# Kernel optimization log

Hardware: AMD Instinct MI355X
Metric: run time of the kernel (lower is better)

Reference implementation:

```python
import jax, jax.numpy as jnp
import numpy as np

TAU = 2.0
BN_EPS = 1e-5
SG_ALPHA = 4.0  # spikingjelly default sigmoid surrogate alpha

@jax.custom_vjp
def heaviside(x):
    return (x >= 0).astype(x.dtype)

def _h_fwd(x):
    return heaviside(x), x

def _h_bwd(x, g):
    sg = jax.nn.sigmoid(SG_ALPHA * x)
    return (SG_ALPHA * sg * (1.0 - sg) * g,)

heaviside.defvjp(_h_fwd, _h_bwd)

def lif(x, v_th):
    # x: (T, ...). LIFNode defaults: tau=2, decay_input=True, v_reset=0 (hard reset).
    def step(v, xt):
        v = v + (xt - v) / TAU
        s = heaviside(v - v_th)
        return v * (1.0 - s), s
    _, spikes = jax.lax.scan(step, jnp.zeros_like(x[0]), x)
    return spikes

def bn(x, gamma, beta, mean, var):
    # x: (T,B,D,V), channel axis = 2; inference-mode BatchNorm1d
    inv = gamma * jax.lax.rsqrt(var + BN_EPS)
    return x * inv[None, None, :, None] + (beta - mean * inv)[None, None, :, None]

def conv1x1(W, x):
    # W: (out,in), x: (T,B,D,V)
    return jnp.einsum('od,tbdv->tbov', W, x)

def setup_inputs() -> dict:
    key = jax.random.key(0)
    T, B, D, V = 4, 64, 512, 256
    ks = jax.random.split(key, 4)
    s = 1.0 / np.sqrt(D)
    return {
        'x': jax.random.normal(ks[0], (T, B, D, V), jnp.float32),
        'Wq': jax.random.normal(ks[1], (D, D), jnp.float32) * s,
        'q_gamma': jnp.ones((D,), jnp.float32), 'q_beta': jnp.zeros((D,), jnp.float32),
        'q_mean': jnp.zeros((D,), jnp.float32), 'q_var': jnp.ones((D,), jnp.float32),
        'Wk': jax.random.normal(ks[2], (D, D), jnp.float32) * s,
        'k_gamma': jnp.ones((D,), jnp.float32), 'k_beta': jnp.zeros((D,), jnp.float32),
        'k_mean': jnp.zeros((D,), jnp.float32), 'k_var': jnp.ones((D,), jnp.float32),
        'Wp': jax.random.normal(ks[3], (D, D), jnp.float32) * s,
        'p_gamma': jnp.ones((D,), jnp.float32), 'p_beta': jnp.zeros((D,), jnp.float32),
        'p_mean': jnp.zeros((D,), jnp.float32), 'p_var': jnp.ones((D,), jnp.float32),
    }

def reference(x, Wq, q_gamma, q_beta, q_mean, q_var,
              Wk, k_gamma, k_beta, k_mean, k_var,
              Wp, p_gamma, p_beta, p_mean, p_var):
    T, B, D, V = x.shape
    H = 4
    hd = D // H
    q = lif(bn(conv1x1(Wq, x), q_gamma, q_beta, q_mean, q_var), 1.0)
    k = lif(bn(conv1x1(Wk, x), k_gamma, k_beta, k_mean, k_var), 1.0)
    qh = q.reshape(T, B, H, hd, V)
    kh = k.reshape(T, B, H, hd, V)
    q_sum = qh.sum(axis=3, keepdims=True)        # (T,B,H,1,V)
    gate = lif(q_sum, 0.5)                        # attn_lif, threshold 0.5
    out = (gate * kh).reshape(T, B, D, V)
    out2 = lif(bn(conv1x1(Wp, out), p_gamma, p_beta, p_mean, p_var), 1.0)
    return out2
```

## Files before the change

### kernel.cpp

```cpp
#include <hip/hip_runtime.h>

#define T_ 4
#define B_ 64
#define D_ 512
#define V_ 256

#define XSH   0ull
#define XSM   67108864ull
#define XSL   134217728ull
#define OUTBT 201326592ull
#define WT    268435456ull
#define BNOF  273154048ull

typedef unsigned short u16;
typedef __attribute__((ext_vector_type(8))) __bf16 bf16x8;
typedef __attribute__((ext_vector_type(4))) float f32x4;
typedef __attribute__((ext_vector_type(8))) unsigned short u16x8;
typedef __attribute__((ext_vector_type(4))) unsigned short u16x4;

__device__ __forceinline__ u16 f2bf(float f) {
    unsigned u = __float_as_uint(f);
    return (u16)((u + 0x7FFFu + ((u >> 16) & 1u)) >> 16);
}
__device__ __forceinline__ float bf2f(u16 h) {
    return __uint_as_float(((unsigned)h) << 16);
}

#define GLL16(g, l) __builtin_amdgcn_global_load_lds( \
    (const __attribute__((address_space(1))) void*)(g), \
    (__attribute__((address_space(3))) void*)(l), 16, 0, 0)
#define WAITVM(n) asm volatile("s_waitcnt vmcnt(" #n ")" ::: "memory")
#define WAITLGKM() asm volatile("s_waitcnt lgkmcnt(0)" ::: "memory")

__global__ __launch_bounds__(256) void k_prep2(
    const float* __restrict__ Wq, const float* __restrict__ Wk, const float* __restrict__ Wp,
    const float* __restrict__ qg, const float* __restrict__ qb,
    const float* __restrict__ qm, const float* __restrict__ qv,
    const float* __restrict__ kg, const float* __restrict__ kb,
    const float* __restrict__ km, const float* __restrict__ kv,
    const float* __restrict__ pg, const float* __restrict__ pb,
    const float* __restrict__ pm, const float* __restrict__ pv,
    char* __restrict__ ws)
{
    const int g = blockIdx.x * 256 + threadIdx.x;
    const int mat = g >> 15;
    const int r = g & 32767;
    const int lane = r & 63;
    const int q = r >> 6;
    const int ip = q & 7;
    const int q2 = q >> 3;
    const int it = q2 & 15;
    const int head = q2 >> 4;
    const int row = head * 128 + ip * 16 + (lane & 15);
    const int kcol = it * 32 + (lane >> 4) * 8;
    const float* W = (mat == 0) ? Wq : (mat == 1 ? Wk : Wp);

    u16x8 h8, m8, l8;
#pragma unroll
    for (int e = 0; e < 8; ++e) {
        const float f = W[row * 512 + kcol + e];
        const u16 h = f2bf(f);          const float fh = bf2f(h);
        const u16 m = f2bf(f - fh);     const float fm = bf2f(m);
        const u16 l = f2bf(f - fh - fm);
        h8[e] = h; m8[e] = m; l8[e] = l;
    }
    u16* wt = (u16*)(ws + WT);
    const size_t o = (size_t)r * 8;
    *(u16x8*)(wt + (size_t)(mat * 3 + 0) * 262144 + o) = h8;
    *(u16x8*)(wt + (size_t)(mat * 3 + 1) * 262144 + o) = m8;
    *(u16x8*)(wt + (size_t)(mat * 3 + 2) * 262144 + o) = l8;

    if (g < 512) {
        float* bn = (float*)(ws + BNOF);
        float iv;
        iv = qg[g] * (1.0f / sqrtf(qv[g] + 1e-5f)); bn[g]        = iv; bn[512  + g] = qb[g] - qm[g] * iv;
        iv = kg[g] * (1.0f / sqrtf(kv[g] + 1e-5f)); bn[1024 + g] = iv; bn[1536 + g] = kb[g] - km[g] * iv;
        iv = pg[g] * (1.0f / sqrtf(pv[g] + 1e-5f)); bn[2048 + g] = iv; bn[2560 + g] = pb[g] - pm[g] * iv;
    }
}

__global__ __launch_bounds__(256) void k_split_x2(
    const float* __restrict__ x, char* __restrict__ ws)
{
    const int bt = blockIdx.x >> 4;
    const int it = blockIdx.x & 15;
    const int tid = threadIdx.x;
#pragma unroll
    for (int r2 = 0; r2 < 4; ++r2) {
        const int slot = r2 * 256 + tid;
        const int vg = slot >> 6;
        const int ll = slot & 63;
        const int v  = vg * 16 + (ll & 15);
        const int d0 = it * 32 + (ll >> 4) * 8;
        u16x8 h8, m8, l8;
#pragma unroll
        for (int e = 0; e < 8; ++e) {
            const float f = x[(size_t)bt * 131072 + (size_t)(d0 + e) * 256 + v];
            const u16 h = f2bf(f);          const float fh = bf2f(h);
            const u16 m = f2bf(f - fh);     const float fm = bf2f(m);
            const u16 lo = f2bf(f - fh - fm);
            h8[e] = h; m8[e] = m; l8[e] = lo;
        }
        const size_t o = (size_t)bt * 262144ull + (size_t)it * 16384ull
                       + (size_t)vg * 1024ull + (size_t)ll * 16ull;
        *(u16x8*)(ws + XSH + o) = h8;
        *(u16x8*)(ws + XSM + o) = m8;
        *(u16x8*)(ws + XSL + o) = l8;
    }
}

__global__ __launch_bounds__(512, 1) void k_qk2(char* __restrict__ ws)
{
    __shared__ char lds[150528];
    float* qs    = (float*)(lds + 147456);
    float* gatef = (float*)(lds + 149504);

    const int tid  = threadIdx.x;
    const int lane = tid & 63;
    const int wave = tid >> 6;
    const int wr = wave >> 2;
    const int wc = wave & 3;
    const int quad = lane >> 4;
    const int l15  = lane & 15;
    const int to   = tid * 16;
    const int offB0 = (wc * 4 + 0 + wr) * 1024 + lane * 16;
    const int offB1 = (wc * 4 + 2 + wr) * 1024 + lane * 16;

    const int xcd  = blockIdx.x & 7;
    const int slot = blockIdx.x >> 3;
    const int b    = xcd * 8 + (slot >> 2);
    const int head = slot & 3;

    constexpr int PA[6] = {0, 0, 1, 1, 0, 2};
    constexpr int PB[6] = {0, 1, 0, 1, 2, 0};

#define QK_ISSUE_A(gg, nb) { \
    const size_t wb_ = WT + (size_t)((gg) >> 6) * 1572864ull \
                     + (size_t)head * 131072ull + (size_t)((gg) & 15) * 8192ull; \
    _Pragma("unroll") \
    for (int s_ = 0; s_ < 3; ++s_) \
        GLL16(ws + wb_ + (size_t)s_ * 524288ull + to, (nb) + s_ * 8192 + to); }

#define QK_ISSUE_B(gg, nb, off) { \
    const size_t bb_ = (size_t)(((((gg) >> 4) & 3) * 64 + b)) * 262144ull \
                     + (size_t)((gg) & 15) * 16384ull; \
    _Pragma("unroll") \
    for (int s_ = 0; s_ < 3; ++s_) \
        GLL16(ws + (size_t)s_ * 67108864ull + bb_ + (off), (nb) + 24576 + s_ * 16384 + (off)); }

#define QK_DO_J(jq) { \
    bf16x8 bfr[3]; \
    _Pragma("unroll") \
    for (int s_ = 0; s_ < 3; ++s_) \
        bfr[s_] = *(const bf16x8*)(buf + 24576 + s_ * 16384 + (wc * 4 + (jq)) * 1024 + lane * 16); \
    __builtin_amdgcn_s_setprio(1); \
    _Pragma("unroll") \
    for (int i_ = 0; i_ < 4; ++i_) \
        _Pragma("unroll") \
        for (int p_ = 0; p_ < 6; ++p_) \
            acc[i_][jq] = __builtin_amdgcn_mfma_f32_16x16x32_bf16( \
                afr[PA[p_]][i_], bfr[PB[p_]], acc[i_][jq], 0, 0, 0); \
    __builtin_amdgcn_s_setprio(0); }

    f32x4 st[4][4], acc[4][4];
    float gstate = 0.f;

    QK_ISSUE_A(0, lds);
    QK_ISSUE_B(0, lds, offB0);
    QK_ISSUE_B(0, lds, offB1);

#pragma unroll 1
    for (int g = 0; g < 128; ++g) {
        const int ph = g >> 6;
        const int t  = (g >> 4) & 3;
        const int it = g & 15;
        char* buf  = lds + (g & 1) * 73728;
        char* nbuf = lds + ((g + 1) & 1) * 73728;
        const bool kepi = (ph == 1) && (it == 15);
        const float* bn = (const float*)(ws + BNOF + (size_t)ph * 4096);

        if (it == 0) {
#pragma unroll
            for (int i = 0; i < 4; ++i)
#pragma unroll
                for (int j = 0; j < 4; ++j) {
                    acc[i][j] = (f32x4){0.f, 0.f, 0.f, 0.f};
                    if (t == 0) st[i][j] = (f32x4){0.f, 0.f, 0.f, 0.f};
                }
        }

        WAITVM(3);
        __builtin_amdgcn_s_barrier();
        if (!kepi) QK_ISSUE_A(g + 1, nbuf);
        bf16x8 afr[3][4];
#pragma unroll
        for (int s = 0; s < 3; ++s)
#pragma unroll
            for (int i = 0; i < 4; ++i)
                afr[s][i] = *(const bf16x8*)(buf + s * 8192 + wr * 4096
                                             + i * 1024 + lane * 16);
        QK_DO_J(0);
        if (!kepi) QK_ISSUE_B(g + 1, nbuf, offB0);
        QK_DO_J(1);
        if (kepi) { WAITVM(0); } else { WAITVM(6); }
        __builtin_amdgcn_s_barrier();
        if (!kepi) QK_ISSUE_B(g + 1, nbuf, offB1);
        QK_DO_J(2);
        QK_DO_J(3);

        if (it == 15) {
            if (ph == 0) {
                float qp[4] = {0.f, 0.f, 0.f, 0.f};
#pragma unroll
                for (int i = 0; i < 4; ++i) {
                    const int ob = head * 128 + wr * 64 + i * 16 + quad * 4;
                    const f32x4 inv = *(const f32x4*)(bn + ob);
                    const f32x4 add = *(const f32x4*)(bn + 512 + ob);
#pragma unroll
                    for (int j = 0; j < 4; ++j)
#pragma unroll
                        for (int r = 0; r < 4; ++r) {
                            const float y = acc[i][j][r] * inv[r] + add[r];
                            float v = (st[i][j][r] + y) * 0.5f;
                            const float s = (v >= 1.0f) ? 1.f : 0.f;
                            st[i][j][r] = (v >= 1.0f) ? 0.f : v;
                            qp[j] += s;
                        }
                }
#pragma unroll
                for (int j = 0; j < 4; ++j) {
                    qp[j] += __shfl_xor(qp[j], 16, 64);
                    qp[j] += __shfl_xor(qp[j], 32, 64);
                }
                if (quad == 0) {
#pragma unroll
                    for (int j = 0; j < 4; ++j)
                        qs[wr * 256 + wc * 64 + j * 16 + l15] = qp[j];
                }
                WAITLGKM();
                __builtin_amdgcn_s_barrier();
                if (tid < 256) {
                    const float qsum = qs[tid] + qs[256 + tid];
                    gstate = (gstate + qsum) * 0.5f;
                    const float gt = (gstate >= 0.5f) ? 1.f : 0.f;
                    gstate = (gstate >= 0.5f) ? 0.f : gstate;
                    gatef[t * 256 + tid] = gt;
                }
                WAITLGKM();
                __builtin_amdgcn_s_barrier();
            } else {
                const int bt = t * 64 + b;
                const size_t dst = OUTBT + ((size_t)bt * 16ull + (size_t)head * 4ull) * 16384ull;
#pragma unroll
                for (int i = 0; i < 4; ++i) {
                    const int ob = head * 128 + wr * 64 + i * 16 + quad * 4;
                    const f32x4 inv = *(const f32x4*)(bn + ob);
                    const f32x4 add = *(const f32x4*)(bn + 512 + ob);
                    const int itL = wr * 2 + (i >> 1);
                    const int ls  = ((i & 1) * 2 + (quad >> 1)) * 16 + l15;
                    const int e0  = (quad & 1) * 4;
#pragma unroll
                    for (int j = 0; j < 4; ++j) {
                        const int col = wc * 64 + j * 16 + l15;
                        const float gt = gatef[t * 256 + col];
                        u16x4 w;
#pragma unroll
                        for (int r = 0; r < 4; ++r) {
                            const float y = acc[i][j][r] * inv[r] + add[r];
                            float v = (st[i][j][r] + y) * 0.5f;
                            const float s = (v >= 1.0f) ? 1.f : 0.f;
                            st[i][j][r] = (v >= 1.0f) ? 0.f : v;
                            w[r] = (s * gt != 0.f) ? (u16)0x3F80 : (u16)0;
                        }
                        *(u16x4*)(ws + dst
                            + (size_t)((itL * 16 + wc * 4 + j) * 64 + ls) * 16 + e0 * 2) = w;
                    }
                }
                if (g != 127) {
                    QK_ISSUE_A(g + 1, nbuf);
                    QK_ISSUE_B(g + 1, nbuf, offB0);
                    QK_ISSUE_B(g + 1, nbuf, offB1);
                }
            }
        }
    }
#undef QK_ISSUE_A
#undef QK_ISSUE_B
#undef QK_DO_J
}

__global__ __launch_bounds__(512, 1) void k_p2(char* __restrict__ ws,
                                               float* __restrict__ out2)
{
    __shared__ char lds[81920];

    const int tid  = threadIdx.x;
    const int lane = tid & 63;
    const int wave = tid >> 6;
    const int wr = wave >> 2;
    const int wc = wave & 3;
    const int quad = lane >> 4;
    const int l15  = lane & 15;
    const int to   = tid * 16;
    const int offB0 = (wc * 4 + 0 + wr) * 1024 + lane * 16;
    const int offB1 = (wc * 4 + 2 + wr) * 1024 + lane * 16;

    const int xcd  = blockIdx.x & 7;
    const int slot = blockIdx.x >> 3;
    const int b  = xcd * 8 + (slot >> 2);
    const int ot = slot & 3;

    const float* bn = (const float*)(ws + BNOF + 8192);

#define P_ISSUE_A(gg, nb) { \
    const size_t wb_ = WT + 6ull * 524288ull + (size_t)ot * 131072ull \
                     + (size_t)((gg) & 15) * 8192ull; \
    _Pragma("unroll") \
    for (int s_ = 0; s_ < 3; ++s_) \
        GLL16(ws + wb_ + (size_t)s_ * 524288ull + to, (nb) + s_ * 8192 + to); }

#define P_ISSUE_B(gg, nb, off) { \
    const size_t bb_ = OUTBT + (size_t)((((gg) >> 4) * 64) + b) * 262144ull \
                     + (size_t)((gg) & 15) * 16384ull; \
    GLL16(ws + bb_ + (off), (nb) + 24576 + (off)); }

#define P_DO_J(jq) { \
    const bf16x8 bfr = *(const bf16x8*)(buf + 24576 + (wc * 4 + (jq)) * 1024 + lane * 16); \
    __builtin_amdgcn_s_setprio(1); \
    _Pragma("unroll") \
    for (int i_ = 0; i_ < 4; ++i_) \
        _Pragma("unroll") \
        for (int p_ = 0; p_ < 3; ++p_) \
            acc[i_][jq] = __builtin_amdgcn_mfma_f32_16x16x32_bf16( \
                afr[p_][i_], bfr, acc[i_][jq], 0, 0, 0); \
    __builtin_amdgcn_s_setprio(0); }

    f32x4 st[4][4], acc[4][4];

    P_ISSUE_A(0, lds);
    P_ISSUE_B(0, lds, offB0);
    P_ISSUE_B(0, lds, offB1);

#pragma unroll 1
    for (int g = 0; g < 64; ++g) {
        const int t  = g >> 4;
        const int it = g & 15;
        char* buf  = lds + (g & 1) * 40960;
        char* nbuf = lds + ((g + 1) & 1) * 40960;
        const bool kepi = (it == 15);

        if (it == 0) {
#pragma unroll
            for (int i = 0; i < 4; ++i)
#pragma unroll
                for (int j = 0; j < 4; ++j) {
                    acc[i][j] = (f32x4){0.f, 0.f, 0.f, 0.f};
                    if (g == 0) st[i][j] = (f32x4){0.f, 0.f, 0.f, 0.f};
                }
        }

        WAITVM(1);
        __builtin_amdgcn_s_barrier();
        if (!kepi) P_ISSUE_A(g + 1, nbuf);
        bf16x8 afr[3][4];
#pragma unroll
        for (int s = 0; s < 3; ++s)
#pragma unroll
            for (int i = 0; i < 4; ++i)
                afr[s][i] = *(const bf16x8*)(buf + s * 8192 + wr * 4096
                                             + i * 1024 + lane * 16);
        P_DO_J(0);
        if (!kepi) P_ISSUE_B(g + 1, nbuf, offB0);
        P_DO_J(1);
        if (kepi) { WAITVM(0); } else { WAITVM(4); }
        __builtin_amdgcn_s_barrier();
        if (!kepi) P_ISSUE_B(g + 1, nbuf, offB1);
        P_DO_J(2);
        P_DO_J(3);

        if (kepi) {
#pragma unroll
            for (int i = 0; i < 4; ++i) {
                const int ob = ot * 128 + wr * 64 + i * 16 + quad * 4;
                const f32x4 inv = *(const f32x4*)(bn + ob);
                const f32x4 add = *(const f32x4*)(bn + 512 + ob);
#pragma unroll
                for (int j = 0; j < 4; ++j) {
                    const int col = wc * 64 + j * 16 + l15;
#pragma unroll
                    for (int r = 0; r < 4; ++r) {
                        const float y = acc[i][j][r] * inv[r] + add[r];
                        float v = (st[i][j][r] + y) * 0.5f;
                        const float s = (v >= 1.0f) ? 1.f : 0.f;
                        st[i][j][r] = (v >= 1.0f) ? 0.f : v;
                        out2[((size_t)(t * 64 + b) * 512 + ob + r) * 256 + col] = s;
                    }
                }
            }
            if (g != 63) {
                P_ISSUE_A(g + 1, nbuf);
                P_ISSUE_B(g + 1, nbuf, offB0);
                P_ISSUE_B(g + 1, nbuf, offB1);
            }
        }
    }
#undef P_ISSUE_A
#undef P_ISSUE_B
#undef P_DO_J
}

extern "C" void kernel_launch(void* const* d_in, const int* in_sizes, int n_in,
                              void* d_out, int out_size, void* d_ws, size_t ws_size,
                              hipStream_t stream)
{
    const float* x  = (const float*)d_in[0];
    const float* Wq = (const float*)d_in[1];
    const float* qg = (const float*)d_in[2];
    const float* qb = (const float*)d_in[3];
    const float* qm = (const float*)d_in[4];
    const float* qv = (const float*)d_in[5];
    const float* Wk = (const float*)d_in[6];
    const float* kg = (const float*)d_in[7];
    const float* kb = (const float*)d_in[8];
    const float* km = (const float*)d_in[9];
    const float* kv = (const float*)d_in[10];
    const float* Wp = (const float*)d_in[11];
    const float* pg = (const float*)d_in[12];
    const float* pb = (const float*)d_in[13];
    const float* pm = (const float*)d_in[14];
    const float* pv = (const float*)d_in[15];

    char* ws = (char*)d_ws;

    k_prep2<<<384, 256, 0, stream>>>(Wq, Wk, Wp, qg, qb, qm, qv,
                                     kg, kb, km, kv, pg, pb, pm, pv, ws);

    k_split_x2<<<4096, 256, 0, stream>>>(x, ws);

    k_qk2<<<256, 512, 0, stream>>>(ws);

    k_p2<<<256, 512, 0, stream>>>(ws, (float*)d_out);
}
```

Baseline: 683.9 us.

## Prefetch next tile during epilogues, stage gated spikes via LDS, drop setprio

The next iteration's A/B loads are now issued during epilogue iterations rather than after the epilogue finishes, so global loads overlap the LIF/BN epilogue work in both the QK and projection kernels. The gated spike output in the QK kernel is first written into the current LDS buffer and then copied to global memory as coalesced 16-byte stores. The s_setprio bracketing around the MFMA groups is removed. The LDS staging adds barriers and reuses the compute buffer while prefetched data goes to the other buffer, which assumes the double-buffer indexing keeps the two apart.

```diff
diff --git a/kernel.cpp b/kernel.cpp
--- a/kernel.cpp
+++ b/kernel.cpp
@@ -31,6 +31,7 @@
     (__attribute__((address_space(3))) void*)(l), 16, 0, 0)
 #define WAITVM(n) asm volatile("s_waitcnt vmcnt(" #n ")" ::: "memory")
 #define WAITLGKM() asm volatile("s_waitcnt lgkmcnt(0)" ::: "memory")
+#define BARRIER_MEM() asm volatile("s_barrier" ::: "memory")
 
 __global__ __launch_bounds__(256) void k_prep2(
     const float* __restrict__ Wq, const float* __restrict__ Wk, const float* __restrict__ Wp,
@@ -153,14 +154,12 @@
     _Pragma("unroll") \
     for (int s_ = 0; s_ < 3; ++s_) \
         bfr[s_] = *(const bf16x8*)(buf + 24576 + s_ * 16384 + (wc * 4 + (jq)) * 1024 + lane * 16); \
-    __builtin_amdgcn_s_setprio(1); \
     _Pragma("unroll") \
     for (int i_ = 0; i_ < 4; ++i_) \
         _Pragma("unroll") \
         for (int p_ = 0; p_ < 6; ++p_) \
             acc[i_][jq] = __builtin_amdgcn_mfma_f32_16x16x32_bf16( \
-                afr[PA[p_]][i_], bfr[PB[p_]], acc[i_][jq], 0, 0, 0); \
-    __builtin_amdgcn_s_setprio(0); }
+                afr[PA[p_]][i_], bfr[PB[p_]], acc[i_][jq], 0, 0, 0); }
 
     f32x4 st[4][4], acc[4][4];
     float gstate = 0.f;
@@ -176,7 +175,7 @@
         const int it = g & 15;
         char* buf  = lds + (g & 1) * 73728;
         char* nbuf = lds + ((g + 1) & 1) * 73728;
-        const bool kepi = (ph == 1) && (it == 15);
+        const bool last = (g == 127);
         const float* bn = (const float*)(ws + BNOF + (size_t)ph * 4096);
 
         if (it == 0) {
@@ -191,7 +190,7 @@
 
         WAITVM(3);
         __builtin_amdgcn_s_barrier();
-        if (!kepi) QK_ISSUE_A(g + 1, nbuf);
+        if (!last) QK_ISSUE_A(g + 1, nbuf);
         bf16x8 afr[3][4];
 #pragma unroll
         for (int s = 0; s < 3; ++s)
@@ -200,11 +199,11 @@
                 afr[s][i] = *(const bf16x8*)(buf + s * 8192 + wr * 4096
                                              + i * 1024 + lane * 16);
         QK_DO_J(0);
-        if (!kepi) QK_ISSUE_B(g + 1, nbuf, offB0);
+        if (!last) QK_ISSUE_B(g + 1, nbuf, offB0);
         QK_DO_J(1);
-        if (kepi) { WAITVM(0); } else { WAITVM(6); }
+        if (last) { WAITVM(0); } else { WAITVM(6); }
         __builtin_amdgcn_s_barrier();
-        if (!kepi) QK_ISSUE_B(g + 1, nbuf, offB1);
+        if (!last) QK_ISSUE_B(g + 1, nbuf, offB1);
         QK_DO_J(2);
         QK_DO_J(3);
 
@@ -249,8 +248,8 @@
                 WAITLGKM();
                 __builtin_amdgcn_s_barrier();
             } else {
-                const int bt = t * 64 + b;
-                const size_t dst = OUTBT + ((size_t)bt * 16ull + (size_t)head * 4ull) * 16384ull;
+                u16* tile = (u16*)buf;
+                BARRIER_MEM();
 #pragma unroll
                 for (int i = 0; i < 4; ++i) {
                     const int ob = head * 128 + wr * 64 + i * 16 + quad * 4;
@@ -272,15 +271,19 @@
                             st[i][j][r] = (v >= 1.0f) ? 0.f : v;
                             w[r] = (s * gt != 0.f) ? (u16)0x3F80 : (u16)0;
                         }
-                        *(u16x4*)(ws + dst
-                            + (size_t)((itL * 16 + wc * 4 + j) * 64 + ls) * 16 + e0 * 2) = w;
+                        *(u16x4*)&tile[(size_t)((itL * 16 + wc * 4 + j) * 64 + ls) * 8 + e0] = w;
                     }
                 }
-                if (g != 127) {
-                    QK_ISSUE_A(g + 1, nbuf);
-                    QK_ISSUE_B(g + 1, nbuf, offB0);
-                    QK_ISSUE_B(g + 1, nbuf, offB1);
-                }
+                WAITLGKM();
+                BARRIER_MEM();
+                const int bt = t * 64 + b;
+                const size_t dst = OUTBT + ((size_t)bt * 16ull + (size_t)head * 4ull) * 16384ull;
+#pragma unroll
+                for (int c = 0; c < 8; ++c) {
+                    const int idx = c * 512 + tid;
+                    *(float4*)(ws + dst + (size_t)idx * 16) = *(const float4*)&tile[(size_t)idx * 8];
+                }
+                BARRIER_MEM();
             }
         }
     }
@@ -326,14 +329,12 @@
 
 #define P_DO_J(jq) { \
     const bf16x8 bfr = *(const bf16x8*)(buf + 24576 + (wc * 4 + (jq)) * 1024 + lane * 16); \
-    __builtin_amdgcn_s_setprio(1); \
     _Pragma("unroll") \
     for (int i_ = 0; i_ < 4; ++i_) \
         _Pragma("unroll") \
         for (int p_ = 0; p_ < 3; ++p_) \
             acc[i_][jq] = __builtin_amdgcn_mfma_f32_16x16x32_bf16( \
-                afr[p_][i_], bfr, acc[i_][jq], 0, 0, 0); \
-    __builtin_amdgcn_s_setprio(0); }
+                afr[p_][i_], bfr, acc[i_][jq], 0, 0, 0); }
 
     f32x4 st[4][4], acc[4][4];
 
@@ -347,7 +348,7 @@
         const int it = g & 15;
         char* buf  = lds + (g & 1) * 40960;
         char* nbuf = lds + ((g + 1) & 1) * 40960;
-        const bool kepi = (it == 15);
+        const bool last = (g == 63);
 
         if (it == 0) {
 #pragma unroll
@@ -361,7 +362,7 @@
 
         WAITVM(1);
         __builtin_amdgcn_s_barrier();
-        if (!kepi) P_ISSUE_A(g + 1, nbuf);
+        if (!last) P_ISSUE_A(g + 1, nbuf);
         bf16x8 afr[3][4];
 #pragma unroll
         for (int s = 0; s < 3; ++s)
@@ -370,15 +371,15 @@
                 afr[s][i] = *(const bf16x8*)(buf + s * 8192 + wr * 4096
                                              + i * 1024 + lane * 16);
         P_DO_J(0);
-        if (!kepi) P_ISSUE_B(g + 1, nbuf, offB0);
+        if (!last) P_ISSUE_B(g + 1, nbuf, offB0);
         P_DO_J(1);
-        if (kepi) { WAITVM(0); } else { WAITVM(4); }
+        if (last) { WAITVM(0); } else { WAITVM(4); }
         __builtin_amdgcn_s_barrier();
-        if (!kepi) P_ISSUE_B(g + 1, nbuf, offB1);
+        if (!last) P_ISSUE_B(g + 1, nbuf, offB1);
         P_DO_J(2);
         P_DO_J(3);
 
-        if (kepi) {
+        if (it == 15) {
 #pragma unroll
             for (int i = 0; i < 4; ++i) {
                 const int ob = ot * 128 + wr * 64 + i * 16 + quad * 4;
@@ -396,11 +397,6 @@
                         out2[((size_t)(t * 64 + b) * 512 + ob + r) * 256 + col] = s;
                     }
                 }
-            }
-            if (g != 63) {
-                P_ISSUE_A(g + 1, nbuf);
-                P_ISSUE_B(g + 1, nbuf, offB0);
-                P_ISSUE_B(g + 1, nbuf, offB1);
             }
         }
     }
```

New measurement: 647.4 us. 5.3% less time.
